# Performance work log

Measured on AMD Instinct MI355X. Metric: run time of the kernel, lower is better.

Reference implementation:

```python
import jax, jax.numpy as jnp
import numpy as np

B, H, W, C = 64, 14, 14, 768

def setup_inputs() -> dict:
    key = jax.random.key(0)
    k = jax.random.split(key, 5)
    s = 0.02  # small init so tanh/sigmoid stay in active range
    return {
        "x": jax.random.normal(k[0], (B, H, W, C), dtype=jnp.float32),
        "Wx": jax.random.normal(k[1], (3 * C, C), dtype=jnp.float32) * s,
        "bx": jnp.zeros((3 * C,), dtype=jnp.float32),
        "Wh": jax.random.normal(k[2], (3 * C, C), dtype=jnp.float32) * s,
        "bh": jnp.zeros((3 * C,), dtype=jnp.float32),
        "Wp": jax.random.normal(k[3], (C, C), dtype=jnp.float32) * s,
    }

def reference(x, Wx, bx, Wh, bh, Wp):
    b, h_, w_, c = x.shape
    n = h_ * w_
    seq = x.reshape(b, n, c)
    # Input projections for all timesteps at once (no recurrent dependency).
    x_zrn = jnp.einsum('bnc,dc->bnd', seq, Wx) + bx  # [B, N, 3C]
    x_zrn_t = jnp.transpose(x_zrn, (1, 0, 2))        # [N, B, 3C] for scan

    def step(h, xz):
        h_zrn = h @ Wh.T + bh                         # [B, 3C]
        x_z, x_r, x_n = jnp.split(xz, 3, axis=-1)
        h_z, h_r, h_n = jnp.split(h_zrn, 3, axis=-1)
        z = jax.nn.sigmoid(x_z + h_z)
        r = jax.nn.sigmoid(x_r + h_r)
        ncand = jnp.tanh(x_n + r * h_n)
        h_new = (1.0 - z) * ncand + z * h
        return h_new, h_new

    h0 = jnp.zeros((b, c), dtype=x.dtype)
    _, hs = jax.lax.scan(step, h0, x_zrn_t)           # hs: [N, B, C]
    y = jnp.transpose(hs, (1, 0, 2))                  # [B, N, C]
    y = jnp.einsum('bnc,dc->bnd', y, Wp)              # proj (no bias)
    # proj_drop = 0.0 -> identity
    return y.reshape(b, h_, w_, c)
```

## Files before the change

### kernel.cpp

```cpp
#include <hip/hip_runtime.h>

typedef unsigned short u16;
typedef unsigned int   u32;
typedef unsigned long long u64;
typedef __attribute__((ext_vector_type(8))) short bf16x8;
typedef __attribute__((ext_vector_type(4))) float f32x4;

#define GK 768
#define NSTEP 196
#define HSTEP 49152
#define PWG 24
#define NBLK 256
#define FLAG0 32
#define MIR0 512

__device__ __forceinline__ u16 f2bf(float f) {
    u32 u = __float_as_uint(f);
    u = (u + 0x7fffu + ((u >> 16) & 1u)) >> 16;
    return (u16)u;
}
__device__ __forceinline__ float bf2f(u16 h) { return __uint_as_float(((u32)h) << 16); }

__global__ __launch_bounds__(256) void cvt_kernel(
    const float4* __restrict__ x, const float4* __restrict__ wx,
    const float4* __restrict__ wp,
    u32* __restrict__ xb, u32* __restrict__ wxb, u32* __restrict__ wpb,
    int* __restrict__ flags)
{
    const int N1 = 9633792 / 4, N2 = 1769472 / 4;
    int i = blockIdx.x * 256 + threadIdx.x;
    if (blockIdx.x == 0) {
        flags[threadIdx.x]       = 0;
        flags[256 + threadIdx.x] = 0;
        flags[512 + threadIdx.x] = 0;
        flags[768 + threadIdx.x] = 0;
    }
    const float4* src; u32* dst; int off;
    if (i < N1)            { src = x;  dst = xb;  off = i; }
    else if (i < N1 + N2)  { src = wx; dst = wxb; off = i - N1; }
    else                   { src = wp; dst = wpb; off = i - N1 - N2; }
    float4 v = src[off];
    u32 lo = (u32)f2bf(v.x) | ((u32)f2bf(v.y) << 16);
    u32 hi = (u32)f2bf(v.z) | ((u32)f2bf(v.w) << 16);
    dst[(size_t)off * 2]     = lo;
    dst[(size_t)off * 2 + 1] = hi;
}

template<int MODE>
__global__ __launch_bounds__(256) void gemm_bt(
    const u16* __restrict__ A, const u16* __restrict__ B,
    const float* __restrict__ bias, void* __restrict__ outv)
{
    __shared__ u16 As[128 * 40];
    __shared__ u16 Bs[128 * 40];
    const int tid  = threadIdx.x;
    const int lane = tid & 63;
    const int wv   = tid >> 6;
    const int m0 = blockIdx.y * 128;
    const int n0 = blockIdx.x * 128;
    const int wm = (wv & 1) * 64;
    const int wn = (wv >> 1) * 64;

    f32x4 acc[4][4];
#pragma unroll
    for (int i = 0; i < 4; ++i)
#pragma unroll
        for (int j = 0; j < 4; ++j) acc[i][j] = (f32x4){0.f, 0.f, 0.f, 0.f};

    const int r0 = tid >> 2, q0 = tid & 3;
    const u16* gA0 = A + (size_t)(m0 + r0)      * GK + q0 * 8;
    const u16* gA1 = A + (size_t)(m0 + r0 + 64) * GK + q0 * 8;
    const u16* gB0 = B + (size_t)(n0 + r0)      * GK + q0 * 8;
    const u16* gB1 = B + (size_t)(n0 + r0 + 64) * GK + q0 * 8;
    u16* sA0 = As + r0 * 40 + q0 * 8;
    u16* sA1 = As + (r0 + 64) * 40 + q0 * 8;
    u16* sB0 = Bs + r0 * 40 + q0 * 8;
    u16* sB1 = Bs + (r0 + 64) * 40 + q0 * 8;

    const int fr = lane & 15, fq = lane >> 4;
    const u16* fA = As + (wm + fr) * 40 + fq * 8;
    const u16* fB = Bs + (wn + fr) * 40 + fq * 8;

    for (int kt = 0; kt < GK / 32; ++kt) {
        uint4 a0 = *(const uint4*)(gA0 + kt * 32);
        uint4 a1 = *(const uint4*)(gA1 + kt * 32);
        uint4 b0 = *(const uint4*)(gB0 + kt * 32);
        uint4 b1 = *(const uint4*)(gB1 + kt * 32);
        __syncthreads();
        *(uint4*)sA0 = a0; *(uint4*)sA1 = a1;
        *(uint4*)sB0 = b0; *(uint4*)sB1 = b1;
        __syncthreads();
        bf16x8 af[4], bfr[4];
#pragma unroll
        for (int mi = 0; mi < 4; ++mi) af[mi]  = *(const bf16x8*)(fA + mi * 16 * 40);
#pragma unroll
        for (int ni = 0; ni < 4; ++ni) bfr[ni] = *(const bf16x8*)(fB + ni * 16 * 40);
#pragma unroll
        for (int mi = 0; mi < 4; ++mi)
#pragma unroll
            for (int ni = 0; ni < 4; ++ni)
                acc[mi][ni] = __builtin_amdgcn_mfma_f32_16x16x32_bf16(
                    af[mi], bfr[ni], acc[mi][ni], 0, 0, 0);
    }

    if (MODE == 1) {
        u16* out = (u16*)outv;
#pragma unroll
        for (int mi = 0; mi < 4; ++mi) {
#pragma unroll
            for (int ni = 0; ni < 4; ++ni) {
                int col = n0 + wn + ni * 16 + fr;
                float bv = bias[col];
#pragma unroll
                for (int r = 0; r < 4; ++r) {
                    int m = m0 + wm + mi * 16 + fq * 4 + r;
                    int b = m / 196;
                    int nn = m - b * 196;
                    u16 hv = f2bf(acc[mi][ni][r] + bv);
                    int other = __shfl_xor((int)hv, 1, 64);
                    if (!(lane & 1)) {
                        u32 packed = (u32)hv | (((u32)(u16)other) << 16);
                        size_t eidx = ((size_t)nn * 64 + (size_t)b) * 2304 + (size_t)col;
                        *((u32*)out + (eidx >> 1)) = packed;
                    }
                }
            }
        }
    } else {
        float* out = (float*)outv;
#pragma unroll
        for (int mi = 0; mi < 4; ++mi) {
#pragma unroll
            for (int ni = 0; ni < 4; ++ni) {
                int col = n0 + wn + ni * 16 + fr;
#pragma unroll
                for (int r = 0; r < 4; ++r) {
                    int m = m0 + wm + mi * 16 + fq * 4 + r;
                    int b = m & 63;
                    int nn = m >> 6;
                    out[((size_t)b * 196 + nn) * 768 + col] = acc[mi][ni][r];
                }
            }
        }
    }
}

__device__ __forceinline__ int poll_load_sc0(const int* p) {
    int v;
    asm volatile("global_load_dword %0, %1, off sc0 nt\n\t"
                 "s_waitcnt vmcnt(0)"
                 : "=v"(v) : "v"(p) : "memory");
    return v;
}
__device__ __forceinline__ void store_sc0(int* p, int v) {
    asm volatile("global_store_dword %0, %1, off sc0"
                 :: "v"(p), "v"(v) : "memory");
}

template<bool LOCAL>
__device__ void recur_run(
    int g, int s, int tid,
    const u16* __restrict__ xz, const float* __restrict__ Wh,
    const float* __restrict__ bh, u16* __restrict__ hsx, int* flags,
    float* hzs)
{
    const int lane = tid & 63;
    const int wv   = tid >> 6;
    const int kh   = wv & 1;
    const int np   = wv >> 1;
    const int fr   = lane & 15, fq = lane >> 4;
    const int c0   = s * 32;
    const int B0   = g * 8;

    bf16x8 bfrag[2][12];
#pragma unroll
    for (int j = 0; j < 2; ++j) {
        int row = np * 768 + c0 + j * 16 + fr;
        const float* wp = Wh + (size_t)row * 768 + kh * 384 + fq * 8;
#pragma unroll
        for (int kk = 0; kk < 12; ++kk) {
            float4 f0 = *(const float4*)(wp + kk * 32);
            float4 f1 = *(const float4*)(wp + kk * 32 + 4);
            bf16x8 b;
            b[0] = (short)f2bf(f0.x); b[1] = (short)f2bf(f0.y);
            b[2] = (short)f2bf(f0.z); b[3] = (short)f2bf(f0.w);
            b[4] = (short)f2bf(f1.x); b[5] = (short)f2bf(f1.y);
            b[6] = (short)f2bf(f1.z); b[7] = (short)f2bf(f1.w);
            bfrag[j][kk] = b;
        }
    }

    const int gb = tid >> 5, gi = tid & 31;
    const int gc = c0 + gi;
    float bh0 = 0.f, bh1 = 0.f, bh2 = 0.f, hold = 0.f;
    if (tid < 256) { bh0 = bh[gc]; bh1 = bh[768 + gc]; bh2 = bh[1536 + gc]; }

    int fl = lane;
    if (fl >= 48) fl -= 48; else if (fl >= 24) fl -= 24;
    int* const myflag      = &flags[FLAG0 + g * 32 + s];
    int* const mymir       = &flags[MIR0  + g * 32 + s];
    const int* const pollf = &flags[FLAG0 + g * 32 + fl];
    const int* const pollm = &flags[MIR0  + g * 32 + fl];

    float xgn0 = 0.f, xgn1 = 0.f, xgn2 = 0.f;
    if (tid < 256) {
        size_t xoff = (size_t)(B0 + gb) * 2304 + gc;
        xgn0 = bf2f(xz[xoff]);
        xgn1 = bf2f(xz[xoff + 768]);
        xgn2 = bf2f(xz[xoff + 1536]);
    }

    bool slow = !LOCAL;

    for (int n = 0; n < NSTEP; ++n) {
        const float xg0 = xgn0, xg1 = xgn1, xg2 = xgn2;

        f32x4 acc0 = (f32x4){0.f, 0.f, 0.f, 0.f};
        f32x4 acc1 = (f32x4){0.f, 0.f, 0.f, 0.f};

        if (n > 0) {
            if (!slow) {
                int tries = 0;
                for (;;) {
                    int v = poll_load_sc0(pollf);
                    if (__all(v >= n)) break;
                    if (++tries > 2048) { slow = true; break; }
                }
            }
            if (slow) {
                const int* pp = LOCAL ? pollm : pollf;
                for (;;) {
                    int v = __hip_atomic_load(pp, __ATOMIC_RELAXED,
                                              __HIP_MEMORY_SCOPE_AGENT);
                    if (__all(v >= n)) break;
                }
            }
            const u16* ap = hsx + (size_t)(n - 1) * HSTEP
                                + (size_t)(B0 + fr) * 768 + kh * 384 + fq * 8;
            const bool arow = fr < 8;
#pragma unroll
            for (int kk = 0; kk < 12; ++kk) {
                bf16x8 a = arow ? *(const bf16x8*)(ap + kk * 32)
                                : (bf16x8){0, 0, 0, 0, 0, 0, 0, 0};
                acc0 = __builtin_amdgcn_mfma_f32_16x16x32_bf16(a, bfrag[0][kk], acc0, 0, 0, 0);
                acc1 = __builtin_amdgcn_mfma_f32_16x16x32_bf16(a, bfrag[1][kk], acc1, 0, 0, 0);
            }
        }

        if (tid < 256) {
            int np1 = (n + 1 < NSTEP) ? n + 1 : NSTEP - 1;
            size_t xoff = ((size_t)np1 * 64 + (B0 + gb)) * 2304 + gc;
            xgn0 = bf2f(xz[xoff]);
            xgn1 = bf2f(xz[xoff + 768]);
            xgn2 = bf2f(xz[xoff + 1536]);
        }

#pragma unroll
        for (int r = 0; r < 4; ++r) {
            int b = fq * 4 + r;
            if (b < 8) {
                hzs[(kh * 8 + b) * 96 + np * 32 + fr]      = acc0[r];
                hzs[(kh * 8 + b) * 96 + np * 32 + 16 + fr] = acc1[r];
            }
        }
        __syncthreads();

        if (tid < 256) {
            float h0 = hzs[gb * 96 + gi]      + hzs[(8 + gb) * 96 + gi]      + bh0;
            float h1 = hzs[gb * 96 + 32 + gi] + hzs[(8 + gb) * 96 + 32 + gi] + bh1;
            float h2 = hzs[gb * 96 + 64 + gi] + hzs[(8 + gb) * 96 + 64 + gi] + bh2;
            float z   = 1.f / (1.f + __expf(-(xg0 + h0)));
            float rr2 = 1.f / (1.f + __expf(-(xg1 + h1)));
            float pre = xg2 + rr2 * h2;
            float e2  = __expf(-2.f * pre);
            float nc  = (1.f - e2) / (1.f + e2);
            float hnew = (1.f - z) * nc + z * hold;
            hold = hnew;

            u16 hv = f2bf(hnew);
            u32 other = ((u32)__shfl_xor((int)hv, 1, 64)) & 0xffffu;
            u32 v01 = (u32)hv | (other << 16);
            u32 v23 = (u32)__shfl_xor((int)v01, 2, 64);
            if ((tid & 3) == 0) {
                u64 q = (u64)v01 | ((u64)v23 << 32);
                size_t ofs = (size_t)n * HSTEP + (size_t)(B0 + gb) * 768 + gc;
                u64* p = (u64*)(hsx + ofs);
                if (LOCAL) {
                    *p = q;
                } else {
                    __hip_atomic_store(p, q, __ATOMIC_RELAXED, __HIP_MEMORY_SCOPE_AGENT);
                }
            }
        }
        asm volatile("s_waitcnt vmcnt(0)" ::: "memory");
        __syncthreads();
        if (LOCAL) {
            if (tid == 0)
                store_sc0(myflag, n + 1);
            else if (tid == 320)
                __hip_atomic_store(mymir, n + 1, __ATOMIC_RELAXED,
                                   __HIP_MEMORY_SCOPE_AGENT);
        } else {
            if (tid == 0)
                __hip_atomic_store(myflag, n + 1, __ATOMIC_RELAXED,
                                   __HIP_MEMORY_SCOPE_AGENT);
        }
    }
}

__global__ __launch_bounds__(384) void recur2_kernel(
    const u16* __restrict__ xz, const float* __restrict__ Wh,
    const float* __restrict__ bh, u16* __restrict__ hsx, int* flags)
{
    __shared__ float hzs[2 * 8 * 96];
    __shared__ int sh_mode, sh_g, sh_s;
    const int tid = threadIdx.x;

    __builtin_amdgcn_fence(__ATOMIC_ACQUIRE, "agent");

    if (tid == 0) {
        u32 xcc = 0;
        asm volatile("s_getreg_b32 %0, hwreg(HW_REG_XCC_ID)" : "=s"(xcc));
        const int my_xcd = (int)(xcc & 7u);
        const int slot = __hip_atomic_fetch_add(&flags[my_xcd], 1, __ATOMIC_ACQ_REL,
                                                __HIP_MEMORY_SCOPE_AGENT);
        __hip_atomic_fetch_add(&flags[15], 1, __ATOMIC_ACQ_REL,
                               __HIP_MEMORY_SCOPE_AGENT);
        while (__hip_atomic_load(&flags[15], __ATOMIC_ACQUIRE,
                                 __HIP_MEMORY_SCOPE_AGENT) < NBLK) {}
        int G = 0, pre = 0, myg = 0;
        for (int x = 0; x < 8; ++x) {
            int c  = __hip_atomic_load(&flags[x], __ATOMIC_RELAXED,
                                       __HIP_MEMORY_SCOPE_AGENT);
            int gx = c / PWG;
            if (x < my_xcd) pre += gx;
            if (x == my_xcd) myg = gx;
            G += gx;
        }
        const int grp = pre + slot / PWG;
        const bool act = (slot < myg * PWG) && (grp < 8);
        sh_mode = (G >= 8) ? (act ? 1 : 2) : 0;
        sh_g = grp;
        sh_s = slot % PWG;
    }
    __syncthreads();
    const int mode = sh_mode;

    if (mode == 1) {
        recur_run<true>(sh_g, sh_s, tid, xz, Wh, bh, hsx, flags, hzs);
    } else if (mode == 0) {
        const int bid = blockIdx.x;
        if (bid < 8 * PWG)
            recur_run<false>(bid & 7, bid >> 3, tid, xz, Wh, bh, hsx, flags, hzs);
    }
}

extern "C" void kernel_launch(void* const* d_in, const int* in_sizes, int n_in,
                              void* d_out, int out_size, void* d_ws, size_t ws_size,
                              hipStream_t stream)
{
    const float* x  = (const float*)d_in[0];
    const float* Wx = (const float*)d_in[1];
    const float* bx = (const float*)d_in[2];
    const float* Wh = (const float*)d_in[3];
    const float* bh = (const float*)d_in[4];
    const float* Wp = (const float*)d_in[5];
    float* out = (float*)d_out;

    char* ws = (char*)d_ws;
    size_t off = 0;
    auto wsalloc = [&](size_t bytes) -> void* {
        void* p = ws + off;
        off += (bytes + 255) & ~(size_t)255;
        return p;
    };
    u16* xb   = (u16*)wsalloc(9633792ull * 2);
    u16* wxb  = (u16*)wsalloc(1769472ull * 2);
    u16* wpb  = (u16*)wsalloc(589824ull * 2);
    u16* xzrn = (u16*)wsalloc(196ull * 64 * 2304 * 2);
    u16* hsx  = (u16*)wsalloc(196ull * 64 * 768 * 2);
    int* flags = (int*)wsalloc(4096);

    cvt_kernel<<<11712, 256, 0, stream>>>(
        (const float4*)x, (const float4*)Wx, (const float4*)Wp,
        (u32*)xb, (u32*)wxb, (u32*)wpb, flags);

    gemm_bt<1><<<dim3(18, 98), 256, 0, stream>>>(xb, wxb, bx, (void*)xzrn);

    {
        const u16* a0 = xzrn; const float* a1 = Wh; const float* a2 = bh;
        u16* a3 = hsx; int* a4 = flags;
        void* args[5] = { &a0, &a1, &a2, &a3, &a4 };
        hipLaunchCooperativeKernel((void*)recur2_kernel, dim3(NBLK), dim3(384),
                                   args, 0, stream);
    }

    gemm_bt<0><<<dim3(6, 98), 256, 0, stream>>>(hsx, wpb, nullptr, (void*)out);
}
```

Before: 1.172 ms.

## Poll step flags from one wave with sleep, and validate sc0 visibility at startup

Per-step polling in the fast path is moved to a single wave that backs off with s_sleep, and the other waves wait at a barrier instead of all spinning. At startup each group runs a sentinel test to confirm that sc0 flag stores are visible to its peers, and falls back to agent-scope atomics if the test fails. Flag polling drops the nt hint, and h stores use explicit sc0 dwordx2 instructions. The aim is to cut cross-XCD polling traffic on the serial recurrence, at the cost of extra barrier and sleep latency on every step, a startup handshake, and fixed clock-based delays on the fallback paths.

```diff
diff --git a/kernel.cpp b/kernel.cpp
--- a/kernel.cpp
+++ b/kernel.cpp
@@ -13,6 +13,7 @@
 #define NBLK 256
 #define FLAG0 32
 #define MIR0 512
+#define SENT (-7777)
 
 __device__ __forceinline__ u16 f2bf(float f) {
     u32 u = __float_as_uint(f);
@@ -147,7 +148,7 @@
 
 __device__ __forceinline__ int poll_load_sc0(const int* p) {
     int v;
-    asm volatile("global_load_dword %0, %1, off sc0 nt\n\t"
+    asm volatile("global_load_dword %0, %1, off sc0\n\t"
                  "s_waitcnt vmcnt(0)"
                  : "=v"(v) : "v"(p) : "memory");
     return v;
@@ -156,8 +157,15 @@
     asm volatile("global_store_dword %0, %1, off sc0"
                  :: "v"(p), "v"(v) : "memory");
 }
-
-template<bool LOCAL>
+__device__ __forceinline__ void store_sc0_u64(u64* p, u64 v) {
+    asm volatile("global_store_dwordx2 %0, %1, off sc0"
+                 :: "v"(p), "v"(v) : "memory");
+}
+__device__ __forceinline__ int agent_load(const int* p) {
+    return __hip_atomic_load(p, __ATOMIC_RELAXED, __HIP_MEMORY_SCOPE_AGENT);
+}
+
+template<bool FAST>
 __device__ void recur_run(
     int g, int s, int tid,
     const u16* __restrict__ xz, const float* __restrict__ Wh,
@@ -210,7 +218,7 @@
         xgn2 = bf2f(xz[xoff + 1536]);
     }
 
-    bool slow = !LOCAL;
+    bool slow = !FAST;
 
     for (int n = 0; n < NSTEP; ++n) {
         const float xg0 = xgn0, xg1 = xgn1, xg2 = xgn2;
@@ -219,19 +227,29 @@
         f32x4 acc1 = (f32x4){0.f, 0.f, 0.f, 0.f};
 
         if (n > 0) {
-            if (!slow) {
-                int tries = 0;
+            if (FAST) {
+                if (tid < 64) {
+                    if (!slow) {
+                        int tries = 0;
+                        for (;;) {
+                            int v = poll_load_sc0(pollf);
+                            if (__all(v >= n)) break;
+                            if (++tries > 1024) { slow = true; break; }
+                            __builtin_amdgcn_s_sleep(1);
+                        }
+                    }
+                    if (slow) {
+                        for (;;) {
+                            int v = agent_load(pollm);
+                            if (__all(v >= n)) break;
+                            __builtin_amdgcn_s_sleep(2);
+                        }
+                    }
+                }
+                __syncthreads();
+            } else {
                 for (;;) {
-                    int v = poll_load_sc0(pollf);
-                    if (__all(v >= n)) break;
-                    if (++tries > 2048) { slow = true; break; }
-                }
-            }
-            if (slow) {
-                const int* pp = LOCAL ? pollm : pollf;
-                for (;;) {
-                    int v = __hip_atomic_load(pp, __ATOMIC_RELAXED,
-                                              __HIP_MEMORY_SCOPE_AGENT);
+                    int v = agent_load(pollf);
                     if (__all(v >= n)) break;
                 }
             }
@@ -285,8 +303,8 @@
                 u64 q = (u64)v01 | ((u64)v23 << 32);
                 size_t ofs = (size_t)n * HSTEP + (size_t)(B0 + gb) * 768 + gc;
                 u64* p = (u64*)(hsx + ofs);
-                if (LOCAL) {
-                    *p = q;
+                if (FAST) {
+                    store_sc0_u64(p, q);
                 } else {
                     __hip_atomic_store(p, q, __ATOMIC_RELAXED, __HIP_MEMORY_SCOPE_AGENT);
                 }
@@ -294,10 +312,10 @@
         }
         asm volatile("s_waitcnt vmcnt(0)" ::: "memory");
         __syncthreads();
-        if (LOCAL) {
+        if (FAST) {
             if (tid == 0)
                 store_sc0(myflag, n + 1);
-            else if (tid == 320)
+            else if (tid == 64)
                 __hip_atomic_store(mymir, n + 1, __ATOMIC_RELAXED,
                                    __HIP_MEMORY_SCOPE_AGENT);
         } else {
@@ -313,7 +331,7 @@
     const float* __restrict__ bh, u16* __restrict__ hsx, int* flags)
 {
     __shared__ float hzs[2 * 8 * 96];
-    __shared__ int sh_mode, sh_g, sh_s;
+    __shared__ int sh_mode, sh_g, sh_s, sh_ok, sh_local;
     const int tid = threadIdx.x;
 
     __builtin_amdgcn_fence(__ATOMIC_ACQUIRE, "agent");
@@ -327,11 +345,11 @@
         __hip_atomic_fetch_add(&flags[15], 1, __ATOMIC_ACQ_REL,
                                __HIP_MEMORY_SCOPE_AGENT);
         while (__hip_atomic_load(&flags[15], __ATOMIC_ACQUIRE,
-                                 __HIP_MEMORY_SCOPE_AGENT) < NBLK) {}
+                                 __HIP_MEMORY_SCOPE_AGENT) < NBLK)
+            __builtin_amdgcn_s_sleep(1);
         int G = 0, pre = 0, myg = 0;
         for (int x = 0; x < 8; ++x) {
-            int c  = __hip_atomic_load(&flags[x], __ATOMIC_RELAXED,
-                                       __HIP_MEMORY_SCOPE_AGENT);
+            int c  = agent_load(&flags[x]);
             int gx = c / PWG;
             if (x < my_xcd) pre += gx;
             if (x == my_xcd) myg = gx;
@@ -345,13 +363,56 @@
     }
     __syncthreads();
     const int mode = sh_mode;
+    const int g = sh_g, s = sh_s;
 
     if (mode == 1) {
-        recur_run<true>(sh_g, sh_s, tid, xz, Wh, bh, hsx, flags, hzs);
+        int* const myflag      = &flags[FLAG0 + g * 32 + s];
+        int fl = tid & 63;
+        if (fl >= 48) fl -= 48; else if (fl >= 24) fl -= 24;
+        const int* const pollf = &flags[FLAG0 + g * 32 + fl];
+
+        if (tid == 0) store_sc0(myflag, SENT);
+        bool stest_ok = false;
+        if (tid < 64) {
+            for (int t = 0; t < 2048; ++t) {
+                int v = poll_load_sc0(pollf);
+                if (__all(v == SENT)) { stest_ok = true; break; }
+                __builtin_amdgcn_s_sleep(1);
+            }
+        }
+        if (tid == 0) {
+            if (!stest_ok)
+                __hip_atomic_fetch_add(&flags[16 + g], 1, __ATOMIC_ACQ_REL,
+                                       __HIP_MEMORY_SCOPE_AGENT);
+            __hip_atomic_fetch_add(&flags[24 + g], 1, __ATOMIC_ACQ_REL,
+                                   __HIP_MEMORY_SCOPE_AGENT);
+            while (agent_load(&flags[24 + g]) < PWG) __builtin_amdgcn_s_sleep(2);
+            sh_local = (agent_load(&flags[16 + g]) == 0) ? 1 : 0;
+            if (g == 0 && s == 0) {
+                bool anyfail = false;
+                for (int x = 0; x < 8; ++x) {
+                    while (agent_load(&flags[24 + x]) < PWG) __builtin_amdgcn_s_sleep(2);
+                    anyfail |= (agent_load(&flags[16 + x]) > 0);
+                }
+                if (anyfail) {
+                    u64 t0 = clock64();
+                    while (clock64() - t0 < 2400000ull) __builtin_amdgcn_s_sleep(8);
+                }
+            }
+        }
+        __syncthreads();
+        if (sh_local)
+            recur_run<true >(g, s, tid, xz, Wh, bh, hsx, flags, hzs);
+        else
+            recur_run<false>(g, s, tid, xz, Wh, bh, hsx, flags, hzs);
     } else if (mode == 0) {
         const int bid = blockIdx.x;
-        if (bid < 8 * PWG)
+        if (bid < 8 * PWG) {
             recur_run<false>(bid & 7, bid >> 3, tid, xz, Wh, bh, hsx, flags, hzs);
+        } else if (bid == NBLK - 1 && tid == 0) {
+            u64 t0 = clock64();
+            while (clock64() - t0 < 4800000ull) __builtin_amdgcn_s_sleep(8);
+        }
     }
 }
 
```

Result: slower. 2.349 ms (+100.4%).

## Simplify recurrence sync: drop XCD-aware group placement, use single-wave polling with barrier

Applied to the files above, without the earlier changes.

Replaces the XCD-aware dynamic block-to-group assignment and the dual-flag fast and slow polling with a static mapping of 192 blocks (8 groups × 24 slices). One wave polls agent-scope flags with s_sleep backoff and a bounded guard, then a block barrier releases the others. The next-step xz prefetch moves after the flag publish. This trades locality-aware L2 sharing within an XCD for a simpler protocol. Cross-XCD flag visibility may add per-step latency, and the guard break could continue before peer data has arrived.

```diff
diff --git a/kernel.cpp b/kernel.cpp
--- a/kernel.cpp
+++ b/kernel.cpp
@@ -10,9 +10,9 @@
 #define NSTEP 196
 #define HSTEP 49152
 #define PWG 24
-#define NBLK 256
-#define FLAG0 32
-#define MIR0 512
+#define NGRP 8
+#define FLINE 32
+#define GUARD (1 << 18)
 
 __device__ __forceinline__ u16 f2bf(float f) {
     u32 u = __float_as_uint(f);
@@ -20,6 +20,13 @@
     return (u16)u;
 }
 __device__ __forceinline__ float bf2f(u16 h) { return __uint_as_float(((u32)h) << 16); }
+
+__device__ __forceinline__ int agent_load(const int* p) {
+    return __hip_atomic_load(p, __ATOMIC_RELAXED, __HIP_MEMORY_SCOPE_AGENT);
+}
+__device__ __forceinline__ void agent_store(int* p, int v) {
+    __hip_atomic_store(p, v, __ATOMIC_RELAXED, __HIP_MEMORY_SCOPE_AGENT);
+}
 
 __global__ __launch_bounds__(256) void cvt_kernel(
     const float4* __restrict__ x, const float4* __restrict__ wx,
@@ -29,12 +36,7 @@
 {
     const int N1 = 9633792 / 4, N2 = 1769472 / 4;
     int i = blockIdx.x * 256 + threadIdx.x;
-    if (blockIdx.x == 0) {
-        flags[threadIdx.x]       = 0;
-        flags[256 + threadIdx.x] = 0;
-        flags[512 + threadIdx.x] = 0;
-        flags[768 + threadIdx.x] = 0;
-    }
+    if (blockIdx.x == 0) flags[threadIdx.x] = 0;
     const float4* src; u32* dst; int off;
     if (i < N1)            { src = x;  dst = xb;  off = i; }
     else if (i < N1 + N2)  { src = wx; dst = wxb; off = i - N1; }
@@ -145,25 +147,15 @@
     }
 }
 
-__device__ __forceinline__ int poll_load_sc0(const int* p) {
-    int v;
-    asm volatile("global_load_dword %0, %1, off sc0 nt\n\t"
-                 "s_waitcnt vmcnt(0)"
-                 : "=v"(v) : "v"(p) : "memory");
-    return v;
-}
-__device__ __forceinline__ void store_sc0(int* p, int v) {
-    asm volatile("global_store_dword %0, %1, off sc0"
-                 :: "v"(p), "v"(v) : "memory");
-}
-
-template<bool LOCAL>
-__device__ void recur_run(
-    int g, int s, int tid,
+__global__ __launch_bounds__(384) void recur3_kernel(
     const u16* __restrict__ xz, const float* __restrict__ Wh,
-    const float* __restrict__ bh, u16* __restrict__ hsx, int* flags,
-    float* hzs)
+    const float* __restrict__ bh, u16* __restrict__ hsx, int* flags)
 {
+    __shared__ float hzs[2 * 8 * 96];
+    const int tid  = threadIdx.x;
+    const int bid  = blockIdx.x;
+    const int g    = bid / PWG;
+    const int s    = bid - g * PWG;
     const int lane = tid & 63;
     const int wv   = tid >> 6;
     const int kh   = wv & 1;
@@ -171,6 +163,8 @@
     const int fr   = lane & 15, fq = lane >> 4;
     const int c0   = s * 32;
     const int B0   = g * 8;
+
+    __builtin_amdgcn_fence(__ATOMIC_ACQUIRE, "agent");
 
     bf16x8 bfrag[2][12];
 #pragma unroll
@@ -195,12 +189,9 @@
     float bh0 = 0.f, bh1 = 0.f, bh2 = 0.f, hold = 0.f;
     if (tid < 256) { bh0 = bh[gc]; bh1 = bh[768 + gc]; bh2 = bh[1536 + gc]; }
 
-    int fl = lane;
-    if (fl >= 48) fl -= 48; else if (fl >= 24) fl -= 24;
-    int* const myflag      = &flags[FLAG0 + g * 32 + s];
-    int* const mymir       = &flags[MIR0  + g * 32 + s];
-    const int* const pollf = &flags[FLAG0 + g * 32 + fl];
-    const int* const pollm = &flags[MIR0  + g * 32 + fl];
+    const int pl = lane % PWG;
+    int* const myflag      = &flags[g * FLINE + s];
+    const int* const pollp = &flags[g * FLINE + pl];
 
     float xgn0 = 0.f, xgn1 = 0.f, xgn2 = 0.f;
     if (tid < 256) {
@@ -210,8 +201,6 @@
         xgn2 = bf2f(xz[xoff + 1536]);
     }
 
-    bool slow = !LOCAL;
-
     for (int n = 0; n < NSTEP; ++n) {
         const float xg0 = xgn0, xg1 = xgn1, xg2 = xgn2;
 
@@ -219,22 +208,17 @@
         f32x4 acc1 = (f32x4){0.f, 0.f, 0.f, 0.f};
 
         if (n > 0) {
-            if (!slow) {
-                int tries = 0;
+            if (tid >= 320) {
+                int guard = 0;
                 for (;;) {
-                    int v = poll_load_sc0(pollf);
+                    int v = agent_load(pollp);
                     if (__all(v >= n)) break;
-                    if (++tries > 2048) { slow = true; break; }
+                    if (++guard > GUARD) break;
+                    __builtin_amdgcn_s_sleep(1);
                 }
             }
-            if (slow) {
-                const int* pp = LOCAL ? pollm : pollf;
-                for (;;) {
-                    int v = __hip_atomic_load(pp, __ATOMIC_RELAXED,
-                                              __HIP_MEMORY_SCOPE_AGENT);
-                    if (__all(v >= n)) break;
-                }
-            }
+            __syncthreads();
+
             const u16* ap = hsx + (size_t)(n - 1) * HSTEP
                                 + (size_t)(B0 + fr) * 768 + kh * 384 + fq * 8;
             const bool arow = fr < 8;
@@ -245,14 +229,6 @@
                 acc0 = __builtin_amdgcn_mfma_f32_16x16x32_bf16(a, bfrag[0][kk], acc0, 0, 0, 0);
                 acc1 = __builtin_amdgcn_mfma_f32_16x16x32_bf16(a, bfrag[1][kk], acc1, 0, 0, 0);
             }
-        }
-
-        if (tid < 256) {
-            int np1 = (n + 1 < NSTEP) ? n + 1 : NSTEP - 1;
-            size_t xoff = ((size_t)np1 * 64 + (B0 + gb)) * 2304 + gc;
-            xgn0 = bf2f(xz[xoff]);
-            xgn1 = bf2f(xz[xoff + 768]);
-            xgn2 = bf2f(xz[xoff + 1536]);
         }
 
 #pragma unroll
@@ -284,74 +260,21 @@
             if ((tid & 3) == 0) {
                 u64 q = (u64)v01 | ((u64)v23 << 32);
                 size_t ofs = (size_t)n * HSTEP + (size_t)(B0 + gb) * 768 + gc;
-                u64* p = (u64*)(hsx + ofs);
-                if (LOCAL) {
-                    *p = q;
-                } else {
-                    __hip_atomic_store(p, q, __ATOMIC_RELAXED, __HIP_MEMORY_SCOPE_AGENT);
-                }
+                __hip_atomic_store((u64*)(hsx + ofs), q,
+                                   __ATOMIC_RELAXED, __HIP_MEMORY_SCOPE_AGENT);
             }
         }
         asm volatile("s_waitcnt vmcnt(0)" ::: "memory");
         __syncthreads();
-        if (LOCAL) {
-            if (tid == 0)
-                store_sc0(myflag, n + 1);
-            else if (tid == 320)
-                __hip_atomic_store(mymir, n + 1, __ATOMIC_RELAXED,
-                                   __HIP_MEMORY_SCOPE_AGENT);
-        } else {
-            if (tid == 0)
-                __hip_atomic_store(myflag, n + 1, __ATOMIC_RELAXED,
-                                   __HIP_MEMORY_SCOPE_AGENT);
-        }
-    }
-}
-
-__global__ __launch_bounds__(384) void recur2_kernel(
-    const u16* __restrict__ xz, const float* __restrict__ Wh,
-    const float* __restrict__ bh, u16* __restrict__ hsx, int* flags)
-{
-    __shared__ float hzs[2 * 8 * 96];
-    __shared__ int sh_mode, sh_g, sh_s;
-    const int tid = threadIdx.x;
-
-    __builtin_amdgcn_fence(__ATOMIC_ACQUIRE, "agent");
-
-    if (tid == 0) {
-        u32 xcc = 0;
-        asm volatile("s_getreg_b32 %0, hwreg(HW_REG_XCC_ID)" : "=s"(xcc));
-        const int my_xcd = (int)(xcc & 7u);
-        const int slot = __hip_atomic_fetch_add(&flags[my_xcd], 1, __ATOMIC_ACQ_REL,
-                                                __HIP_MEMORY_SCOPE_AGENT);
-        __hip_atomic_fetch_add(&flags[15], 1, __ATOMIC_ACQ_REL,
-                               __HIP_MEMORY_SCOPE_AGENT);
-        while (__hip_atomic_load(&flags[15], __ATOMIC_ACQUIRE,
-                                 __HIP_MEMORY_SCOPE_AGENT) < NBLK) {}
-        int G = 0, pre = 0, myg = 0;
-        for (int x = 0; x < 8; ++x) {
-            int c  = __hip_atomic_load(&flags[x], __ATOMIC_RELAXED,
-                                       __HIP_MEMORY_SCOPE_AGENT);
-            int gx = c / PWG;
-            if (x < my_xcd) pre += gx;
-            if (x == my_xcd) myg = gx;
-            G += gx;
-        }
-        const int grp = pre + slot / PWG;
-        const bool act = (slot < myg * PWG) && (grp < 8);
-        sh_mode = (G >= 8) ? (act ? 1 : 2) : 0;
-        sh_g = grp;
-        sh_s = slot % PWG;
-    }
-    __syncthreads();
-    const int mode = sh_mode;
-
-    if (mode == 1) {
-        recur_run<true>(sh_g, sh_s, tid, xz, Wh, bh, hsx, flags, hzs);
-    } else if (mode == 0) {
-        const int bid = blockIdx.x;
-        if (bid < 8 * PWG)
-            recur_run<false>(bid & 7, bid >> 3, tid, xz, Wh, bh, hsx, flags, hzs);
+        if (tid == 0) agent_store(myflag, n + 1);
+
+        if (tid < 256) {
+            int np1 = (n + 1 < NSTEP) ? n + 1 : NSTEP - 1;
+            size_t xoff = ((size_t)np1 * 64 + (B0 + gb)) * 2304 + gc;
+            xgn0 = bf2f(xz[xoff]);
+            xgn1 = bf2f(xz[xoff + 768]);
+            xgn2 = bf2f(xz[xoff + 1536]);
+        }
     }
 }
 
@@ -379,7 +302,7 @@
     u16* wpb  = (u16*)wsalloc(589824ull * 2);
     u16* xzrn = (u16*)wsalloc(196ull * 64 * 2304 * 2);
     u16* hsx  = (u16*)wsalloc(196ull * 64 * 768 * 2);
-    int* flags = (int*)wsalloc(4096);
+    int* flags = (int*)wsalloc(1024);
 
     cvt_kernel<<<11712, 256, 0, stream>>>(
         (const float4*)x, (const float4*)Wx, (const float4*)Wp,
@@ -391,8 +314,8 @@
         const u16* a0 = xzrn; const float* a1 = Wh; const float* a2 = bh;
         u16* a3 = hsx; int* a4 = flags;
         void* args[5] = { &a0, &a1, &a2, &a3, &a4 };
-        hipLaunchCooperativeKernel((void*)recur2_kernel, dim3(NBLK), dim3(384),
-                                   args, 0, stream);
+        hipLaunchCooperativeKernel((void*)recur3_kernel, dim3(NGRP * PWG),
+                                   dim3(384), args, 0, stream);
     }
 
     gemm_bt<0><<<dim3(6, 98), 256, 0, stream>>>(hsx, wpb, nullptr, (void*)out);
```

Result: faster. 1.096 ms (-6.5%).
